# Kernel optimization log

Hardware: AMD Instinct MI355X
Metric: run time of the kernel (lower is better)

## Reference

```python
import jax, jax.numpy as jnp
import numpy as np

N, E = 32768, 524288
MUL = 32        # multiplicity of 0e and 1o in hidden irreps
N_ATTR = 4      # node attr scalars (species one-hot)
N_RAD = 8       # radial basis size
FC_H = 64       # radial MLP hidden width
AVG_NEIGH = 16.0
INV3 = 1.0 / np.sqrt(3.0)  # w3j(1,1,0) contraction coefficient


def setup_inputs() -> dict:
    key = jax.random.key(0)
    ks = jax.random.split(key, 16)
    p = lambda k, s: jax.random.normal(k, s, dtype=jnp.float32)
    return {
        "node_feats": p(ks[0], (N, MUL + 3 * MUL)),
        "node_attrs": jax.random.uniform(ks[1], (N, N_ATTR), dtype=jnp.float32),
        "edge_feats": p(ks[2], (E, N_RAD)),
        "edge_attrs": p(ks[3], (E, 4)),
        "W1s": p(ks[4], (MUL, MUL)),
        "W1v": p(ks[5], (MUL, MUL)),
        "Wf1": p(ks[6], (N_RAD, FC_H)),
        "Wf2": p(ks[7], (FC_H, FC_H)),
        "Wf3": p(ks[8], (FC_H, 4 * MUL)),
        "W2s": p(ks[9], (2 * MUL, 2 * MUL)),
        "W2v": p(ks[10], (2 * MUL, MUL)),
        "Wsc_s": p(ks[11], (MUL, N_ATTR, 2 * MUL)),
        "Wsc_v": p(ks[12], (MUL, N_ATTR, MUL)),
        "edge_index": jax.random.randint(ks[13], (2, E), 0, N),
    }


def reference(node_feats, node_attrs, edge_feats, edge_attrs,
              W1s, W1v, Wf1, Wf2, Wf3, W2s, W2v, Wsc_s, Wsc_v, edge_index):
    silu = jax.nn.silu
    sender, receiver = edge_index[0], edge_index[1]
    xs0 = node_feats[:, :MUL]                      # [N, MUL]   0e scalars
    xv0 = node_feats[:, MUL:].reshape(-1, MUL, 3)  # [N, MUL, 3] 1o vectors

    # linear_1 (irrep-wise, e3nn fan-in normalization)
    xs = (xs0 @ W1s) / np.sqrt(MUL)
    xv = jnp.einsum('nui,uv->nvi', xv0, W1v) / np.sqrt(MUL)

    # radial MLP -> per-edge tensor-product weights
    h = silu((edge_feats @ Wf1) / np.sqrt(N_RAD))
    h = silu((h @ Wf2) / np.sqrt(FC_H))
    w = (h @ Wf3) / np.sqrt(FC_H)                  # [E, 4*MUL]
    w0, w1, w2, w3 = jnp.split(w, 4, axis=1)       # [E, MUL] each

    sh0 = edge_attrs[:, :1]                        # [E, 1]  l=0
    sh1 = edge_attrs[:, 1:4]                       # [E, 3]  l=1
    xs_e = xs[sender]                              # [E, MUL]
    xv_e = xv[sender]                              # [E, MUL, 3]

    # per-edge 'uvu' tensor product paths (only paths landing in 0e/1o kept)
    m_s0 = w0 * xs_e * sh0                                      # 0e x 0e -> 0e
    m_s1 = w3 * jnp.einsum('eui,ei->eu', xv_e, sh1) * INV3      # 1o x 1o -> 0e
    m_v0 = (w1 * xs_e)[:, :, None] * sh1[:, None, :]            # 0e x 1o -> 1o
    m_v1 = (w2 * sh0)[:, :, None] * xv_e                        # 1o x 0e -> 1o

    msg_s = jnp.concatenate([m_s0, m_s1], axis=1)               # [E, 2*MUL]
    msg_v = jnp.concatenate([m_v0, m_v1], axis=1)               # [E, 2*MUL, 3]

    # scatter-add message passing, normalized by avg num neighbours
    agg_s = jax.ops.segment_sum(msg_s, receiver, num_segments=N) / AVG_NEIGH
    agg_v = jax.ops.segment_sum(msg_v, receiver, num_segments=N) / AVG_NEIGH

    # linear_2 to conv output irreps (2*MUL x 0e + MUL x 1o)
    out_s = (agg_s @ W2s) / np.sqrt(2 * MUL)                    # [N, 2*MUL]
    out_v = jnp.einsum('nui,uv->nvi', agg_v, W2v) / np.sqrt(2 * MUL)

    # self connection: FullyConnectedTensorProduct(x_in, node_attrs)
    norm_sc = 1.0 / np.sqrt(MUL * N_ATTR)
    out_s = out_s + jnp.einsum('nu,na,uaw->nw', xs0, node_attrs, Wsc_s) * norm_sc
    out_v = out_v + jnp.einsum('nui,na,uaw->nwi', xv0, node_attrs, Wsc_v) * norm_sc

    # Gate nonlinearity: act(scalars) ++ act(gates) * gated vectors
    scalars = silu(out_s[:, :MUL])
    gates = silu(out_s[:, MUL:])
    gated = out_v * gates[:, :, None]
    new_feats = jnp.concatenate([scalars, gated.reshape(-1, 3 * MUL)], axis=1)

    # resnet add (irreps_layer_out == interaction_irreps_in)
    return node_feats + new_feats
```

## Files before the change

kernel.cpp:

```cpp
#include <hip/hip_runtime.h>
#include <hip/hip_bf16.h>

#define NN 32768
#define NE 524288

typedef __attribute__((ext_vector_type(8))) short short8v;
typedef __attribute__((ext_vector_type(4))) short short4v;
typedef __attribute__((ext_vector_type(4))) float f32x4;
typedef __attribute__((ext_vector_type(4))) float f32x4v;
typedef __attribute__((ext_vector_type(4))) unsigned u32x4;

__device__ __forceinline__ float silu_f(float x){ return x * (1.0f/(1.0f+__expf(-x))); }
__device__ __forceinline__ float bf2f(unsigned short u){ return __uint_as_float(((unsigned)u)<<16); }
__device__ __forceinline__ unsigned short f2bf(float f){
  __hip_bfloat16 b = __float2bfloat16(f);
  return __builtin_bit_cast(unsigned short, b);
}
__device__ __forceinline__ unsigned pk2(float lo, float hi){
  return (unsigned)f2bf(lo) | ((unsigned)f2bf(hi) << 16);
}

#define S32 0.17677669529663687f
#define S8  0.35355339059327373f
#define S64 0.125f
#define R16 0.0625f
#define NSC 0.08838834764831845f
#define INV3F 0.5773502691896258f

__global__ void k_zero(int* __restrict__ deg){
  deg[blockIdx.x*256 + threadIdx.x] = 0;
}

__global__ void k_hist(const int* __restrict__ eidx, int* __restrict__ deg){
  int e = blockIdx.x*256 + threadIdx.x;
  int r = eidx[NE + e];
  atomicAdd(&deg[r], 1);
}

__global__ void __launch_bounds__(1024) k_scan(const int* __restrict__ deg,
    int* __restrict__ row_start, int* __restrict__ cursor){
  __shared__ int lds[1024];
  int t = threadIdx.x;
  int4 v[8];
  const int4* dg = reinterpret_cast<const int4*>(deg) + t*8;
  int s = 0;
  #pragma unroll
  for (int j=0;j<8;j++){ v[j] = dg[j]; s += v[j].x+v[j].y+v[j].z+v[j].w; }
  lds[t] = s; __syncthreads();
  for (int off=1; off<1024; off<<=1){
    int q = (t>=off)? lds[t-off] : 0; __syncthreads();
    lds[t] += q; __syncthreads();
  }
  int run = (t==0)?0:lds[t-1];
  int4* rs = reinterpret_cast<int4*>(row_start) + t*8;
  int4* cu = reinterpret_cast<int4*>(cursor) + t*8;
  #pragma unroll
  for (int j=0;j<8;j++){
    int4 o;
    o.x = run; run += v[j].x;
    o.y = run; run += v[j].y;
    o.z = run; run += v[j].z;
    o.w = run; run += v[j].w;
    rs[j] = o; cu[j] = o;
  }
  if (t==1023) row_start[NN] = run;
}

__global__ void k_scatter(const int* __restrict__ eidx, int* __restrict__ cursor,
                          int* __restrict__ eperm, int* __restrict__ sperm){
  int e = blockIdx.x*256 + threadIdx.x;
  int r = eidx[NE + e];
  int s = eidx[e];
  int pos = atomicAdd(&cursor[r], 1);
  eperm[pos] = e;
  sperm[pos] = s;
}

#define XT_ITERS 16
__global__ void __launch_bounds__(256) k_xt(const float* __restrict__ nf,
    const float* __restrict__ W1s, const float* __restrict__ W1v,
    float* __restrict__ xtp2){
  __shared__ float rowbuf[256];
  int t = threadIdx.x;
  int c = t & 127, u = c >> 2, comp = c & 3;
  int node = t >> 7;
  const float* W = (comp==0) ? W1s : W1v;
  float wreg[32];
  #pragma unroll
  for (int k=0;k<32;k++) wreg[k] = W[k*32 + u];
  int soff = node*128 + (comp==0 ? 0 : 32 + (comp-1));
  int stride = (comp==0) ? 1 : 3;
  int base = blockIdx.x * (2*XT_ITERS);
  #pragma unroll 1
  for (int it=0; it<XT_ITERS; it++){
    int n0 = base + it*2;
    __syncthreads();
    rowbuf[t] = nf[(size_t)n0*128 + t];
    __syncthreads();
    float acc = 0.f;
    #pragma unroll
    for (int k=0;k<32;k++) acc += rowbuf[soff + k*stride] * wreg[k];
    xtp2[(size_t)(n0+node)*128 + c] = acc * S32;
  }
}

__global__ void k_wprep(const float* __restrict__ Wf1, const float* __restrict__ Wf2,
                        const float* __restrict__ Wf3,
                        const float* __restrict__ W2s, const float* __restrict__ W2v,
                        const float* __restrict__ Wsc_s, const float* __restrict__ Wsc_v,
                        short* __restrict__ wfrag, short* __restrict__ wfe){
  int f = blockIdx.x;
  int l = threadIdx.x;
  int c = l & 15, g = l >> 4;
  short8v pk;
  if (f < 28){
    #pragma unroll
    for (int j=0;j<8;j++){
      int k = ((j&4) ? 16 : 0) + g*4 + (j&3);
      float val;
      if (f < 4){
        int m = f;
        val = (k < 8) ? Wf1[k*64 + m*16 + c]*S8 : 0.f;
      } else if (f < 12){
        int idx = f-4, m = idx>>1, kk = idx&1;
        val = Wf2[(kk*32+k)*64 + m*16 + c]*S64;
      } else {
        int idx = f-12, m = idx>>1, kk = idx&1;
        val = Wf3[(kk*32+k)*128 + m*16 + c]*S64;
        if (m >= 6) val *= INV3F;
      }
      pk[j] = (short)f2bf(val);
    }
    reinterpret_cast<short8v*>(wfrag)[f*64 + l] = pk;
  } else {
    int fe = f - 28, kb = fe/6, p = fe%6;
    #pragma unroll
    for (int j=0;j<8;j++){
      int k = kb*32 + ((j&4) ? 16 : 0) + g*4 + (j&3);
      float val;
      if (p < 4){
        int col = p*16 + c;
        val = (k < 64) ? W2s[k*64 + col]*S64 : Wsc_s[(k-64)*64 + col]*NSC;
      } else {
        int col = (p-4)*16 + c;
        val = (k < 64) ? W2v[k*32 + col]*S64 : Wsc_v[(k-64)*32 + col]*NSC;
      }
      pk[j] = (short)f2bf(val);
    }
    reinterpret_cast<short8v*>(wfe)[fe*64 + l] = pk;
  }
}

__global__ void __launch_bounds__(256) k_mlp2(const float* __restrict__ ef,
    const float* __restrict__ ea, const int* __restrict__ eperm,
    const short* __restrict__ wfrag, unsigned* __restrict__ wpair,
    float* __restrict__ shp){
  int lane = threadIdx.x & 63;
  int wv = threadIdx.x >> 6;
  int tile = blockIdx.x*4 + wv;
  int e_l = lane & 15, g = lane >> 4;
  const short8v* wf = reinterpret_cast<const short8v*>(wfrag);

  int pos = tile*16 + e_l;
  int e = eperm[pos];
  if (lane < 16){
    f32x4v av = *reinterpret_cast<const f32x4v*>(ea + (size_t)e*4);
    __builtin_nontemporal_store(av, reinterpret_cast<f32x4v*>(shp + (size_t)pos*4));
  }

  short8v bx = {};
  if (lane < 32){
    const float4 xv = *reinterpret_cast<const float4*>(ef + (size_t)e*8 + g*4);
    bx[0]=(short)f2bf(xv.x); bx[1]=(short)f2bf(xv.y);
    bx[2]=(short)f2bf(xv.z); bx[3]=(short)f2bf(xv.w);
  }
  f32x4 a1[4];
  #pragma unroll
  for (int m=0;m<4;m++){
    f32x4 z = {};
    a1[m] = __builtin_amdgcn_mfma_f32_16x16x32_bf16(wf[m*64+lane], bx, z, 0,0,0);
  }
  short8v b2[2];
  #pragma unroll
  for (int m=0;m<4;m++)
    #pragma unroll
    for (int r=0;r<4;r++)
      b2[m>>1][(m&1)*4 + r] = (short)f2bf(silu_f(a1[m][r]));
  f32x4 a2[4] = {};
  #pragma unroll
  for (int kk=0;kk<2;kk++)
    #pragma unroll
    for (int m=0;m<4;m++)
      a2[m] = __builtin_amdgcn_mfma_f32_16x16x32_bf16(wf[(4+2*m+kk)*64+lane], b2[kk], a2[m], 0,0,0);
  short8v b3[2];
  #pragma unroll
  for (int m=0;m<4;m++)
    #pragma unroll
    for (int r=0;r<4;r++)
      b3[m>>1][(m&1)*4 + r] = (short)f2bf(silu_f(a2[m][r]));
  f32x4 a3[8] = {};
  #pragma unroll
  for (int kk=0;kk<2;kk++)
    #pragma unroll
    for (int m=0;m<8;m++)
      a3[m] = __builtin_amdgcn_mfma_f32_16x16x32_bf16(wf[(12+2*m+kk)*64+lane], b3[kk], a3[m], 0,0,0);
  unsigned* dst = wpair + (size_t)tile*1024 + e_l*64;
  #pragma unroll
  for (int mm=0; mm<2; mm++){
    u32x4 o;
    o.x = pk2(a3[mm][0], a3[mm+2][0]);
    o.y = pk2(a3[mm][1], a3[mm+2][1]);
    o.z = pk2(a3[mm][2], a3[mm+2][2]);
    o.w = pk2(a3[mm][3], a3[mm+2][3]);
    __builtin_nontemporal_store(o, reinterpret_cast<u32x4*>(dst + mm*16 + g*4));
    u32x4 o2;
    o2.x = pk2(a3[6+mm][0], a3[4+mm][0]);
    o2.y = pk2(a3[6+mm][1], a3[4+mm][1]);
    o2.z = pk2(a3[6+mm][2], a3[4+mm][2]);
    o2.w = pk2(a3[6+mm][3], a3[4+mm][3]);
    __builtin_nontemporal_store(o2, reinterpret_cast<u32x4*>(dst + 32 + mm*16 + g*4));
  }
}

#define RV_NODES 4
__global__ void __launch_bounds__(256) k_recv(
    const float* __restrict__ shp, const int* __restrict__ row_start,
    const int* __restrict__ sperm, const unsigned* __restrict__ wpair,
    const float* __restrict__ xtp2, unsigned* __restrict__ agg){
  int wv = threadIdx.x >> 6;
  int lane = threadIdx.x & 63;
  int u = lane & 31;
  bool h1 = lane >= 32;
  bool even = (lane & 1) == 0;
  int nbase = (blockIdx.x*4 + wv) * RV_NODES;

#define EDGE_BODY(WP, SH, Q)                                         \
  {                                                                  \
    float wA = bf2f((unsigned short)((WP) & 0xffffu));               \
    float wB = bf2f((unsigned short)((WP) >> 16));                   \
    float x0 = h1 ? (Q).y : (Q).x;                                   \
    float x1 = h1 ? (Q).z : (Q).x;                                   \
    float x2 = h1 ? (Q).w : (Q).x;                                   \
    float c0 = h1 ? (SH).y : (SH).x;                                 \
    float c1 = h1 ? (SH).z : 0.f;                                    \
    float c2 = h1 ? (SH).w : 0.f;                                    \
    a0 += wA*(x0*c0 + x1*c1 + x2*c2);                                \
    float g0 = wB*(h1 ? (SH).x : (SH).y);                            \
    float g1 = wB*(h1 ? (SH).x : (SH).z);                            \
    float g2 = wB*(h1 ? (SH).x : (SH).w);                            \
    a1 += g0*x0; a2 += g1*x1; a3 += g2*x2;                           \
  }

  #pragma unroll 1
  for (int nn=0; nn<RV_NODES; nn++){
    int n = nbase + nn;
    int lo = row_start[n], hi = row_start[n+1];
    float a0=0.f, a1=0.f, a2=0.f, a3=0.f;
    int idx = lo;
    for (; idx+4 <= hi; idx += 4){
      int s0 = sperm[idx+0], s1 = sperm[idx+1];
      int s2 = sperm[idx+2], s3 = sperm[idx+3];
      unsigned wp0 = __builtin_nontemporal_load(&wpair[(size_t)(idx+0)*64 + lane]);
      unsigned wp1 = __builtin_nontemporal_load(&wpair[(size_t)(idx+1)*64 + lane]);
      unsigned wp2 = __builtin_nontemporal_load(&wpair[(size_t)(idx+2)*64 + lane]);
      unsigned wp3 = __builtin_nontemporal_load(&wpair[(size_t)(idx+3)*64 + lane]);
      f32x4v sh0 = __builtin_nontemporal_load(reinterpret_cast<const f32x4v*>(shp + (size_t)(idx+0)*4));
      f32x4v sh1 = __builtin_nontemporal_load(reinterpret_cast<const f32x4v*>(shp + (size_t)(idx+1)*4));
      f32x4v sh2 = __builtin_nontemporal_load(reinterpret_cast<const f32x4v*>(shp + (size_t)(idx+2)*4));
      f32x4v sh3 = __builtin_nontemporal_load(reinterpret_cast<const f32x4v*>(shp + (size_t)(idx+3)*4));
      int b0 = __builtin_amdgcn_readfirstlane(s0);
      int b1 = __builtin_amdgcn_readfirstlane(s1);
      int b2 = __builtin_amdgcn_readfirstlane(s2);
      int b3 = __builtin_amdgcn_readfirstlane(s3);
      f32x4v q0 = *reinterpret_cast<const f32x4v*>(xtp2 + (size_t)b0*128 + u*4);
      f32x4v q1 = *reinterpret_cast<const f32x4v*>(xtp2 + (size_t)b1*128 + u*4);
      f32x4v q2 = *reinterpret_cast<const f32x4v*>(xtp2 + (size_t)b2*128 + u*4);
      f32x4v q3 = *reinterpret_cast<const f32x4v*>(xtp2 + (size_t)b3*128 + u*4);
      EDGE_BODY(wp0, sh0, q0);
      EDGE_BODY(wp1, sh1, q1);
      EDGE_BODY(wp2, sh2, q2);
      EDGE_BODY(wp3, sh3, q3);
    }
    for (; idx < hi; ++idx){
      int sb = __builtin_amdgcn_readfirstlane(sperm[idx]);
      unsigned wp = __builtin_nontemporal_load(&wpair[(size_t)idx*64 + lane]);
      f32x4v sh = __builtin_nontemporal_load(reinterpret_cast<const f32x4v*>(shp + (size_t)idx*4));
      f32x4v q = *reinterpret_cast<const f32x4v*>(xtp2 + (size_t)sb*128 + u*4);
      EDGE_BODY(wp, sh, q);
    }
    float p0 = __shfl_xor(a0, 1);
    float p1 = __shfl_xor(a1, 1);
    float p2 = __shfl_xor(a2, 1);
    float p3 = __shfl_xor(a3, 1);
    if (even){
      unsigned* ag = agg + (size_t)n*128 + (lane>>1);
      ag[0]  = pk2(a0*R16, p0*R16);
      ag[32] = pk2(a1*R16, p1*R16);
      ag[64] = pk2(a2*R16, p2*R16);
      ag[96] = pk2(a3*R16, p3*R16);
    }
  }
#undef EDGE_BODY
}

__global__ void __launch_bounds__(256) k_epi(
    const float* __restrict__ nf, const float* __restrict__ na,
    const unsigned short* __restrict__ agg, const short* __restrict__ wfe,
    float* __restrict__ out){
  __shared__ float L[4][16][168];
  int wv = threadIdx.x >> 6, lane = threadIdx.x & 63;
  int tile = blockIdx.x*4 + wv;
  int e = lane & 15, g = lane >> 4;
  int n = tile*16 + e;
  const short8v* WE = reinterpret_cast<const short8v*>(wfe);
  const unsigned short* ag = agg + (size_t)n*256;
  const float* nfr = nf + (size_t)n*128;
  float4 nav = *reinterpret_cast<const float4*>(na + (size_t)n*4);

  f32x4 as0={},as1={},as2={},as3={};
  f32x4 av00={},av01={},av10={},av11={},av20={},av21={};

  #pragma unroll
  for (int kb=0; kb<6; kb++){
    short8v bs, bv0, bv1, bv2;
    if (kb < 2){
      int k0 = kb*32 + g*4;
      #pragma unroll
      for (int i=0;i<4;i++){
        short4v qa = *reinterpret_cast<const short4v*>(ag + i*64 + k0);
        short4v qb = *reinterpret_cast<const short4v*>(ag + i*64 + k0 + 16);
        short8v b;
        b[0]=qa[0]; b[1]=qa[1]; b[2]=qa[2]; b[3]=qa[3];
        b[4]=qb[0]; b[5]=qb[1]; b[6]=qb[2]; b[7]=qb[3];
        if (i==0) bs = b; else if (i==1) bv0 = b; else if (i==2) bv1 = b; else bv2 = b;
      }
    } else {
      int u0 = (kb-2)*8 + g;
      float x0 = nfr[u0], x1 = nfr[u0+4];
      bs[0]=(short)f2bf(x0*nav.x); bs[1]=(short)f2bf(x0*nav.y);
      bs[2]=(short)f2bf(x0*nav.z); bs[3]=(short)f2bf(x0*nav.w);
      bs[4]=(short)f2bf(x1*nav.x); bs[5]=(short)f2bf(x1*nav.y);
      bs[6]=(short)f2bf(x1*nav.z); bs[7]=(short)f2bf(x1*nav.w);
      #pragma unroll
      for (int i=0;i<3;i++){
        float y0 = nfr[32 + u0*3 + i], y1 = nfr[32 + (u0+4)*3 + i];
        short8v b;
        b[0]=(short)f2bf(y0*nav.x); b[1]=(short)f2bf(y0*nav.y);
        b[2]=(short)f2bf(y0*nav.z); b[3]=(short)f2bf(y0*nav.w);
        b[4]=(short)f2bf(y1*nav.x); b[5]=(short)f2bf(y1*nav.y);
        b[6]=(short)f2bf(y1*nav.z); b[7]=(short)f2bf(y1*nav.w);
        if (i==0) bv0 = b; else if (i==1) bv1 = b; else bv2 = b;
      }
    }
    as0 = __builtin_amdgcn_mfma_f32_16x16x32_bf16(WE[(kb*6+0)*64+lane], bs, as0, 0,0,0);
    as1 = __builtin_amdgcn_mfma_f32_16x16x32_bf16(WE[(kb*6+1)*64+lane], bs, as1, 0,0,0);
    as2 = __builtin_amdgcn_mfma_f32_16x16x32_bf16(WE[(kb*6+2)*64+lane], bs, as2, 0,0,0);
    as3 = __builtin_amdgcn_mfma_f32_16x16x32_bf16(WE[(kb*6+3)*64+lane], bs, as3, 0,0,0);
    av00 = __builtin_amdgcn_mfma_f32_16x16x32_bf16(WE[(kb*6+4)*64+lane], bv0, av00, 0,0,0);
    av01 = __builtin_amdgcn_mfma_f32_16x16x32_bf16(WE[(kb*6+5)*64+lane], bv0, av01, 0,0,0);
    av10 = __builtin_amdgcn_mfma_f32_16x16x32_bf16(WE[(kb*6+4)*64+lane], bv1, av10, 0,0,0);
    av11 = __builtin_amdgcn_mfma_f32_16x16x32_bf16(WE[(kb*6+5)*64+lane], bv1, av11, 0,0,0);
    av20 = __builtin_amdgcn_mfma_f32_16x16x32_bf16(WE[(kb*6+4)*64+lane], bv2, av20, 0,0,0);
    av21 = __builtin_amdgcn_mfma_f32_16x16x32_bf16(WE[(kb*6+5)*64+lane], bv2, av21, 0,0,0);
  }

  float (*Lw)[168] = L[wv];
  #pragma unroll
  for (int r=0;r<4;r++){
    Lw[e][ 0 + g*4 + r] = silu_f(as0[r]);
    Lw[e][16 + g*4 + r] = silu_f(as1[r]);
    Lw[e][32 + g*4 + r] = silu_f(as2[r]);
    Lw[e][48 + g*4 + r] = silu_f(as3[r]);
    Lw[e][64 + (     g*4 + r)*3 + 0] = av00[r];
    Lw[e][64 + (16 + g*4 + r)*3 + 0] = av01[r];
    Lw[e][64 + (     g*4 + r)*3 + 1] = av10[r];
    Lw[e][64 + (16 + g*4 + r)*3 + 1] = av11[r];
    Lw[e][64 + (     g*4 + r)*3 + 2] = av20[r];
    Lw[e][64 + (16 + g*4 + r)*3 + 2] = av21[r];
  }
  __syncthreads();

  if (g == 0){
    #pragma unroll
    for (int c=0;c<32;c+=4){
      float4 nv = *reinterpret_cast<const float4*>(nfr + c);
      float4 o;
      o.x = nv.x + Lw[e][c  ];
      o.y = nv.y + Lw[e][c+1];
      o.z = nv.z + Lw[e][c+2];
      o.w = nv.w + Lw[e][c+3];
      *reinterpret_cast<float4*>(out + (size_t)n*128 + c) = o;
    }
  } else {
    int q0 = (g-1)*32;
    #pragma unroll
    for (int q=q0; q<q0+32; q+=4){
      float4 nv = *reinterpret_cast<const float4*>(nfr + 32 + q);
      float4 o;
      o.x = nv.x + Lw[e][64+q+0]*Lw[e][32+(q+0)/3];
      o.y = nv.y + Lw[e][64+q+1]*Lw[e][32+(q+1)/3];
      o.z = nv.z + Lw[e][64+q+2]*Lw[e][32+(q+2)/3];
      o.w = nv.w + Lw[e][64+q+3]*Lw[e][32+(q+3)/3];
      *reinterpret_cast<float4*>(out + (size_t)n*128 + 32 + q) = o;
    }
  }
}

extern "C" void kernel_launch(void* const* d_in, const int* in_sizes, int n_in,
                              void* d_out, int out_size, void* d_ws, size_t ws_size,
                              hipStream_t stream) {
  const float* nf    = (const float*)d_in[0];
  const float* na    = (const float*)d_in[1];
  const float* ef    = (const float*)d_in[2];
  const float* ea    = (const float*)d_in[3];
  const float* W1s   = (const float*)d_in[4];
  const float* W1v   = (const float*)d_in[5];
  const float* Wf1   = (const float*)d_in[6];
  const float* Wf2   = (const float*)d_in[7];
  const float* Wf3   = (const float*)d_in[8];
  const float* W2s   = (const float*)d_in[9];
  const float* W2v   = (const float*)d_in[10];
  const float* Wsc_s = (const float*)d_in[11];
  const float* Wsc_v = (const float*)d_in[12];
  const int*   eidx  = (const int*)d_in[13];
  float* out = (float*)d_out;

  char* ws = (char*)d_ws;
  size_t off = 0;
  auto alloc = [&](size_t bytes)->void*{
    void* p = ws + off; off += (bytes + 255) & ~(size_t)255; return p;
  };
  float*    xtp2      = (float*)alloc((size_t)NN*128*4);
  unsigned* wpair     = (unsigned*)alloc((size_t)NE*64*4);
  unsigned* agg       = (unsigned*)alloc((size_t)NN*256*2);
  float*    shp       = (float*)alloc((size_t)NE*16);
  int*      deg       = (int*)alloc((size_t)NN*4);
  int*      row_start = (int*)alloc((size_t)(NN+16)*4);
  int*      cursor    = (int*)alloc((size_t)NN*4);
  int*      eperm     = (int*)alloc((size_t)NE*4);
  int*      sperm     = (int*)alloc((size_t)NE*4);
  short*    wfrag     = (short*)alloc((size_t)28*64*8*2);
  short*    wfe       = (short*)alloc((size_t)36*64*8*2);
  if (off > ws_size) return;

  k_zero   <<<NN/256, 256, 0, stream>>>(deg);
  k_hist   <<<NE/256, 256, 0, stream>>>(eidx, deg);
  k_scan   <<<1, 1024, 0, stream>>>(deg, row_start, cursor);
  k_scatter<<<NE/256, 256, 0, stream>>>(eidx, cursor, eperm, sperm);
  k_xt     <<<NN/(2*XT_ITERS), 256, 0, stream>>>(nf, W1s, W1v, xtp2);
  k_wprep  <<<64, 64, 0, stream>>>(Wf1, Wf2, Wf3, W2s, W2v, Wsc_s, Wsc_v, wfrag, wfe);
  k_mlp2   <<<8192, 256, 0, stream>>>(ef, ea, eperm, wfrag, wpair, shp);
  k_recv   <<<NN/(4*RV_NODES), 256, 0, stream>>>(shp, row_start, sperm, wpair, xtp2,
                                      (unsigned*)agg);
  k_epi    <<<512, 256, 0, stream>>>(nf, na, (const unsigned short*)agg, wfe, out);
}
```

Baseline: 254.8 us.

## Fuse radial MLP into receiver aggregation with 16-padded CSR rows

Removes the separate per-edge MLP kernel and its large bf16 weight buffer and sh copy in global memory. The aggregation kernel now pads each receiver's edge list to a multiple of 16, computes the radial MLP per 16-edge tile with MFMA, stages the results in LDS and consumes them directly. This avoids writing and re-reading the per-edge weights, which is about 128 MB of traffic. In exchange, padding adds wasted MFMA work for low-degree nodes, extra fill kernels are launched, and warps that own nodes of very different degree become imbalanced.

```diff
diff --git a/kernel.cpp b/kernel.cpp
--- a/kernel.cpp
+++ b/kernel.cpp
@@ -3,6 +3,7 @@
 
 #define NN 32768
 #define NE 524288
+#define PADCAP (NE + 16*NN)
 
 typedef __attribute__((ext_vector_type(8))) short short8v;
 typedef __attribute__((ext_vector_type(4))) short short4v;
@@ -27,8 +28,11 @@
 #define NSC 0.08838834764831845f
 #define INV3F 0.5773502691896258f
 
-__global__ void k_zero(int* __restrict__ deg){
-  deg[blockIdx.x*256 + threadIdx.x] = 0;
+__global__ void k_zero(int* __restrict__ p){
+  p[blockIdx.x*256 + threadIdx.x] = 0;
+}
+__global__ void k_fillm1(int* __restrict__ p){
+  p[blockIdx.x*256 + threadIdx.x] = -1;
 }
 
 __global__ void k_hist(const int* __restrict__ eidx, int* __restrict__ deg){
@@ -38,21 +42,26 @@
 }
 
 __global__ void __launch_bounds__(1024) k_scan(const int* __restrict__ deg,
-    int* __restrict__ row_start, int* __restrict__ cursor){
+    int* __restrict__ rs_pad, int* __restrict__ cursor){
   __shared__ int lds[1024];
   int t = threadIdx.x;
   int4 v[8];
   const int4* dg = reinterpret_cast<const int4*>(deg) + t*8;
   int s = 0;
   #pragma unroll
-  for (int j=0;j<8;j++){ v[j] = dg[j]; s += v[j].x+v[j].y+v[j].z+v[j].w; }
+  for (int j=0;j<8;j++){
+    v[j] = dg[j];
+    v[j].x = (v[j].x+15)&~15; v[j].y = (v[j].y+15)&~15;
+    v[j].z = (v[j].z+15)&~15; v[j].w = (v[j].w+15)&~15;
+    s += v[j].x+v[j].y+v[j].z+v[j].w;
+  }
   lds[t] = s; __syncthreads();
   for (int off=1; off<1024; off<<=1){
     int q = (t>=off)? lds[t-off] : 0; __syncthreads();
     lds[t] += q; __syncthreads();
   }
   int run = (t==0)?0:lds[t-1];
-  int4* rs = reinterpret_cast<int4*>(row_start) + t*8;
+  int4* rs = reinterpret_cast<int4*>(rs_pad) + t*8;
   int4* cu = reinterpret_cast<int4*>(cursor) + t*8;
   #pragma unroll
   for (int j=0;j<8;j++){
@@ -63,7 +72,7 @@
     o.w = run; run += v[j].w;
     rs[j] = o; cu[j] = o;
   }
-  if (t==1023) row_start[NN] = run;
+  if (t==1023) rs_pad[NN] = run;
 }
 
 __global__ void k_scatter(const int* __restrict__ eidx, int* __restrict__ cursor,
@@ -151,142 +160,132 @@
   }
 }
 
-__global__ void __launch_bounds__(256) k_mlp2(const float* __restrict__ ef,
-    const float* __restrict__ ea, const int* __restrict__ eperm,
-    const short* __restrict__ wfrag, unsigned* __restrict__ wpair,
-    float* __restrict__ shp){
-  int lane = threadIdx.x & 63;
-  int wv = threadIdx.x >> 6;
-  int tile = blockIdx.x*4 + wv;
-  int e_l = lane & 15, g = lane >> 4;
-  const short8v* wf = reinterpret_cast<const short8v*>(wfrag);
-
-  int pos = tile*16 + e_l;
-  int e = eperm[pos];
-  if (lane < 16){
-    f32x4v av = *reinterpret_cast<const f32x4v*>(ea + (size_t)e*4);
-    __builtin_nontemporal_store(av, reinterpret_cast<f32x4v*>(shp + (size_t)pos*4));
-  }
-
-  short8v bx = {};
-  if (lane < 32){
-    const float4 xv = *reinterpret_cast<const float4*>(ef + (size_t)e*8 + g*4);
-    bx[0]=(short)f2bf(xv.x); bx[1]=(short)f2bf(xv.y);
-    bx[2]=(short)f2bf(xv.z); bx[3]=(short)f2bf(xv.w);
-  }
-  f32x4 a1[4];
-  #pragma unroll
-  for (int m=0;m<4;m++){
-    f32x4 z = {};
-    a1[m] = __builtin_amdgcn_mfma_f32_16x16x32_bf16(wf[m*64+lane], bx, z, 0,0,0);
-  }
-  short8v b2[2];
-  #pragma unroll
-  for (int m=0;m<4;m++)
-    #pragma unroll
-    for (int r=0;r<4;r++)
-      b2[m>>1][(m&1)*4 + r] = (short)f2bf(silu_f(a1[m][r]));
-  f32x4 a2[4] = {};
-  #pragma unroll
-  for (int kk=0;kk<2;kk++)
-    #pragma unroll
-    for (int m=0;m<4;m++)
-      a2[m] = __builtin_amdgcn_mfma_f32_16x16x32_bf16(wf[(4+2*m+kk)*64+lane], b2[kk], a2[m], 0,0,0);
-  short8v b3[2];
-  #pragma unroll
-  for (int m=0;m<4;m++)
-    #pragma unroll
-    for (int r=0;r<4;r++)
-      b3[m>>1][(m&1)*4 + r] = (short)f2bf(silu_f(a2[m][r]));
-  f32x4 a3[8] = {};
-  #pragma unroll
-  for (int kk=0;kk<2;kk++)
-    #pragma unroll
-    for (int m=0;m<8;m++)
-      a3[m] = __builtin_amdgcn_mfma_f32_16x16x32_bf16(wf[(12+2*m+kk)*64+lane], b3[kk], a3[m], 0,0,0);
-  unsigned* dst = wpair + (size_t)tile*1024 + e_l*64;
-  #pragma unroll
-  for (int mm=0; mm<2; mm++){
-    u32x4 o;
-    o.x = pk2(a3[mm][0], a3[mm+2][0]);
-    o.y = pk2(a3[mm][1], a3[mm+2][1]);
-    o.z = pk2(a3[mm][2], a3[mm+2][2]);
-    o.w = pk2(a3[mm][3], a3[mm+2][3]);
-    __builtin_nontemporal_store(o, reinterpret_cast<u32x4*>(dst + mm*16 + g*4));
-    u32x4 o2;
-    o2.x = pk2(a3[6+mm][0], a3[4+mm][0]);
-    o2.y = pk2(a3[6+mm][1], a3[4+mm][1]);
-    o2.z = pk2(a3[6+mm][2], a3[4+mm][2]);
-    o2.w = pk2(a3[6+mm][3], a3[4+mm][3]);
-    __builtin_nontemporal_store(o2, reinterpret_cast<u32x4*>(dst + 32 + mm*16 + g*4));
-  }
-}
-
-#define RV_NODES 4
-__global__ void __launch_bounds__(256) k_recv(
-    const float* __restrict__ shp, const int* __restrict__ row_start,
-    const int* __restrict__ sperm, const unsigned* __restrict__ wpair,
+#define RV_NODES 2
+__global__ void __launch_bounds__(256) k_fused(
+    const float* __restrict__ ef, const float* __restrict__ ea,
+    const int* __restrict__ rs_pad, const int* __restrict__ eperm,
+    const int* __restrict__ sperm, const short* __restrict__ wfrag,
     const float* __restrict__ xtp2, unsigned* __restrict__ agg){
+  __shared__ unsigned sb[4][16][68];
+  __shared__ __align__(16) float shs[4][16][4];
   int wv = threadIdx.x >> 6;
   int lane = threadIdx.x & 63;
+  int e_l = lane & 15, g = lane >> 4;
   int u = lane & 31;
   bool h1 = lane >= 32;
   bool even = (lane & 1) == 0;
+  const short8v* wf = reinterpret_cast<const short8v*>(wfrag);
+  unsigned (*SB)[68] = sb[wv];
+  float (*SH)[4] = shs[wv];
   int nbase = (blockIdx.x*4 + wv) * RV_NODES;
 
-#define EDGE_BODY(WP, SH, Q)                                         \
+#define EDGE_BODY(WP, SH4, Q)                                        \
   {                                                                  \
     float wA = bf2f((unsigned short)((WP) & 0xffffu));               \
     float wB = bf2f((unsigned short)((WP) >> 16));                   \
     float x0 = h1 ? (Q).y : (Q).x;                                   \
     float x1 = h1 ? (Q).z : (Q).x;                                   \
     float x2 = h1 ? (Q).w : (Q).x;                                   \
-    float c0 = h1 ? (SH).y : (SH).x;                                 \
-    float c1 = h1 ? (SH).z : 0.f;                                    \
-    float c2 = h1 ? (SH).w : 0.f;                                    \
+    float c0 = h1 ? (SH4).y : (SH4).x;                               \
+    float c1 = h1 ? (SH4).z : 0.f;                                   \
+    float c2 = h1 ? (SH4).w : 0.f;                                   \
     a0 += wA*(x0*c0 + x1*c1 + x2*c2);                                \
-    float g0 = wB*(h1 ? (SH).x : (SH).y);                            \
-    float g1 = wB*(h1 ? (SH).x : (SH).z);                            \
-    float g2 = wB*(h1 ? (SH).x : (SH).w);                            \
+    float g0 = wB*(h1 ? (SH4).x : (SH4).y);                          \
+    float g1 = wB*(h1 ? (SH4).x : (SH4).z);                          \
+    float g2 = wB*(h1 ? (SH4).x : (SH4).w);                          \
     a1 += g0*x0; a2 += g1*x1; a3 += g2*x2;                           \
   }
 
   #pragma unroll 1
   for (int nn=0; nn<RV_NODES; nn++){
     int n = nbase + nn;
-    int lo = row_start[n], hi = row_start[n+1];
+    int lo = rs_pad[n], hi = rs_pad[n+1];
     float a0=0.f, a1=0.f, a2=0.f, a3=0.f;
-    int idx = lo;
-    for (; idx+4 <= hi; idx += 4){
-      int s0 = sperm[idx+0], s1 = sperm[idx+1];
-      int s2 = sperm[idx+2], s3 = sperm[idx+3];
-      unsigned wp0 = __builtin_nontemporal_load(&wpair[(size_t)(idx+0)*64 + lane]);
-      unsigned wp1 = __builtin_nontemporal_load(&wpair[(size_t)(idx+1)*64 + lane]);
-      unsigned wp2 = __builtin_nontemporal_load(&wpair[(size_t)(idx+2)*64 + lane]);
-      unsigned wp3 = __builtin_nontemporal_load(&wpair[(size_t)(idx+3)*64 + lane]);
-      f32x4v sh0 = __builtin_nontemporal_load(reinterpret_cast<const f32x4v*>(shp + (size_t)(idx+0)*4));
-      f32x4v sh1 = __builtin_nontemporal_load(reinterpret_cast<const f32x4v*>(shp + (size_t)(idx+1)*4));
-      f32x4v sh2 = __builtin_nontemporal_load(reinterpret_cast<const f32x4v*>(shp + (size_t)(idx+2)*4));
-      f32x4v sh3 = __builtin_nontemporal_load(reinterpret_cast<const f32x4v*>(shp + (size_t)(idx+3)*4));
-      int b0 = __builtin_amdgcn_readfirstlane(s0);
-      int b1 = __builtin_amdgcn_readfirstlane(s1);
-      int b2 = __builtin_amdgcn_readfirstlane(s2);
-      int b3 = __builtin_amdgcn_readfirstlane(s3);
-      f32x4v q0 = *reinterpret_cast<const f32x4v*>(xtp2 + (size_t)b0*128 + u*4);
-      f32x4v q1 = *reinterpret_cast<const f32x4v*>(xtp2 + (size_t)b1*128 + u*4);
-      f32x4v q2 = *reinterpret_cast<const f32x4v*>(xtp2 + (size_t)b2*128 + u*4);
-      f32x4v q3 = *reinterpret_cast<const f32x4v*>(xtp2 + (size_t)b3*128 + u*4);
-      EDGE_BODY(wp0, sh0, q0);
-      EDGE_BODY(wp1, sh1, q1);
-      EDGE_BODY(wp2, sh2, q2);
-      EDGE_BODY(wp3, sh3, q3);
-    }
-    for (; idx < hi; ++idx){
-      int sb = __builtin_amdgcn_readfirstlane(sperm[idx]);
-      unsigned wp = __builtin_nontemporal_load(&wpair[(size_t)idx*64 + lane]);
-      f32x4v sh = __builtin_nontemporal_load(reinterpret_cast<const f32x4v*>(shp + (size_t)idx*4));
-      f32x4v q = *reinterpret_cast<const f32x4v*>(xtp2 + (size_t)sb*128 + u*4);
-      EDGE_BODY(wp, sh, q);
+
+    #pragma unroll 1
+    for (int tp = lo; tp < hi; tp += 16){
+      int e = eperm[tp + e_l];
+      int ec = e < 0 ? 0 : e;
+      if (lane < 16){
+        f32x4v av = {0.f,0.f,0.f,0.f};
+        if (e >= 0) av = *reinterpret_cast<const f32x4v*>(ea + (size_t)ec*4);
+        *reinterpret_cast<f32x4v*>(SH[e_l]) = av;
+      }
+      short8v bx = {};
+      if (lane < 32){
+        const float4 xv = *reinterpret_cast<const float4*>(ef + (size_t)ec*8 + g*4);
+        bx[0]=(short)f2bf(xv.x); bx[1]=(short)f2bf(xv.y);
+        bx[2]=(short)f2bf(xv.z); bx[3]=(short)f2bf(xv.w);
+      }
+      f32x4 a1f[4];
+      #pragma unroll
+      for (int m=0;m<4;m++){
+        f32x4 z = {};
+        a1f[m] = __builtin_amdgcn_mfma_f32_16x16x32_bf16(wf[m*64+lane], bx, z, 0,0,0);
+      }
+      short8v b2[2];
+      #pragma unroll
+      for (int m=0;m<4;m++)
+        #pragma unroll
+        for (int r=0;r<4;r++)
+          b2[m>>1][(m&1)*4 + r] = (short)f2bf(silu_f(a1f[m][r]));
+      f32x4 a2f[4] = {};
+      #pragma unroll
+      for (int kk=0;kk<2;kk++)
+        #pragma unroll
+        for (int m=0;m<4;m++)
+          a2f[m] = __builtin_amdgcn_mfma_f32_16x16x32_bf16(wf[(4+2*m+kk)*64+lane], b2[kk], a2f[m], 0,0,0);
+      short8v b3[2];
+      #pragma unroll
+      for (int m=0;m<4;m++)
+        #pragma unroll
+        for (int r=0;r<4;r++)
+          b3[m>>1][(m&1)*4 + r] = (short)f2bf(silu_f(a2f[m][r]));
+      f32x4 a3f[8] = {};
+      #pragma unroll
+      for (int kk=0;kk<2;kk++)
+        #pragma unroll
+        for (int m=0;m<8;m++)
+          a3f[m] = __builtin_amdgcn_mfma_f32_16x16x32_bf16(wf[(12+2*m+kk)*64+lane], b3[kk], a3f[m], 0,0,0);
+      #pragma unroll
+      for (int mm=0; mm<2; mm++){
+        u32x4 o;
+        o.x = pk2(a3f[mm][0], a3f[mm+2][0]);
+        o.y = pk2(a3f[mm][1], a3f[mm+2][1]);
+        o.z = pk2(a3f[mm][2], a3f[mm+2][2]);
+        o.w = pk2(a3f[mm][3], a3f[mm+2][3]);
+        *reinterpret_cast<u32x4*>(&SB[e_l][mm*16 + g*4]) = o;
+        u32x4 o2;
+        o2.x = pk2(a3f[6+mm][0], a3f[4+mm][0]);
+        o2.y = pk2(a3f[6+mm][1], a3f[4+mm][1]);
+        o2.z = pk2(a3f[6+mm][2], a3f[4+mm][2]);
+        o2.w = pk2(a3f[6+mm][3], a3f[4+mm][3]);
+        *reinterpret_cast<u32x4*>(&SB[e_l][32 + mm*16 + g*4]) = o2;
+      }
+      #pragma unroll 1
+      for (int jq=0; jq<4; jq++){
+        int4 sA = *reinterpret_cast<const int4*>(sperm + tp + jq*4);
+        unsigned wp0 = SB[jq*4+0][lane];
+        unsigned wp1 = SB[jq*4+1][lane];
+        unsigned wp2 = SB[jq*4+2][lane];
+        unsigned wp3 = SB[jq*4+3][lane];
+        f32x4v sh0 = *reinterpret_cast<const f32x4v*>(SH[jq*4+0]);
+        f32x4v sh1 = *reinterpret_cast<const f32x4v*>(SH[jq*4+1]);
+        f32x4v sh2 = *reinterpret_cast<const f32x4v*>(SH[jq*4+2]);
+        f32x4v sh3 = *reinterpret_cast<const f32x4v*>(SH[jq*4+3]);
+        int b0 = __builtin_amdgcn_readfirstlane(sA.x);
+        int b1 = __builtin_amdgcn_readfirstlane(sA.y);
+        int b2i = __builtin_amdgcn_readfirstlane(sA.z);
+        int b3i = __builtin_amdgcn_readfirstlane(sA.w);
+        f32x4v q0 = *reinterpret_cast<const f32x4v*>(xtp2 + (size_t)b0*128 + u*4);
+        f32x4v q1 = *reinterpret_cast<const f32x4v*>(xtp2 + (size_t)b1*128 + u*4);
+        f32x4v q2 = *reinterpret_cast<const f32x4v*>(xtp2 + (size_t)b2i*128 + u*4);
+        f32x4v q3 = *reinterpret_cast<const f32x4v*>(xtp2 + (size_t)b3i*128 + u*4);
+        EDGE_BODY(wp0, sh0, q0);
+        EDGE_BODY(wp1, sh1, q1);
+        EDGE_BODY(wp2, sh2, q2);
+        EDGE_BODY(wp3, sh3, q3);
+      }
     }
     float p0 = __shfl_xor(a0, 1);
     float p1 = __shfl_xor(a1, 1);
@@ -431,26 +430,25 @@
     void* p = ws + off; off += (bytes + 255) & ~(size_t)255; return p;
   };
   float*    xtp2      = (float*)alloc((size_t)NN*128*4);
-  unsigned* wpair     = (unsigned*)alloc((size_t)NE*64*4);
   unsigned* agg       = (unsigned*)alloc((size_t)NN*256*2);
-  float*    shp       = (float*)alloc((size_t)NE*16);
   int*      deg       = (int*)alloc((size_t)NN*4);
-  int*      row_start = (int*)alloc((size_t)(NN+16)*4);
+  int*      rs_pad    = (int*)alloc((size_t)(NN+16)*4);
   int*      cursor    = (int*)alloc((size_t)NN*4);
-  int*      eperm     = (int*)alloc((size_t)NE*4);
-  int*      sperm     = (int*)alloc((size_t)NE*4);
+  int*      eperm     = (int*)alloc((size_t)PADCAP*4);
+  int*      sperm     = (int*)alloc((size_t)PADCAP*4);
   short*    wfrag     = (short*)alloc((size_t)28*64*8*2);
   short*    wfe       = (short*)alloc((size_t)36*64*8*2);
   if (off > ws_size) return;
 
   k_zero   <<<NN/256, 256, 0, stream>>>(deg);
+  k_fillm1 <<<PADCAP/256, 256, 0, stream>>>(eperm);
+  k_zero   <<<PADCAP/256, 256, 0, stream>>>(sperm);
   k_hist   <<<NE/256, 256, 0, stream>>>(eidx, deg);
-  k_scan   <<<1, 1024, 0, stream>>>(deg, row_start, cursor);
+  k_scan   <<<1, 1024, 0, stream>>>(deg, rs_pad, cursor);
   k_scatter<<<NE/256, 256, 0, stream>>>(eidx, cursor, eperm, sperm);
   k_xt     <<<NN/(2*XT_ITERS), 256, 0, stream>>>(nf, W1s, W1v, xtp2);
   k_wprep  <<<64, 64, 0, stream>>>(Wf1, Wf2, Wf3, W2s, W2v, Wsc_s, Wsc_v, wfrag, wfe);
-  k_mlp2   <<<8192, 256, 0, stream>>>(ef, ea, eperm, wfrag, wpair, shp);
-  k_recv   <<<NN/(4*RV_NODES), 256, 0, stream>>>(shp, row_start, sperm, wpair, xtp2,
-                                      (unsigned*)agg);
+  k_fused  <<<NN/(4*RV_NODES), 256, 0, stream>>>(ef, ea, rs_pad, eperm, sperm,
+                                                 wfrag, xtp2, (unsigned*)agg);
   k_epi    <<<512, 256, 0, stream>>>(nf, na, (const unsigned short*)agg, wfe, out);
 }
```

New measurement: 431.4 us. 69.3% more time.
